# Kernel optimization log

Measured on AMD Instinct MI355X. Metric: run time of the kernel, lower is better.

## Reference

```python
import jax, jax.numpy as jnp
import numpy as np

SEQ_LEN = 4096
EMBED_DIM = 1280
NUM_HEADS = 16
HEAD_DIM = EMBED_DIM // NUM_HEADS  # 80
SCALING = float(np.sqrt(HEAD_DIM))  # NOTE: source multiplies by sqrt(head_dim)
NEG_INF = float(np.finfo(np.float32).min)


def rotate_half(x):
    x1, x2 = jnp.split(x, 2, axis=-1)
    return jnp.concatenate((-x2, x1), axis=-1)


def setup_inputs() -> dict:
    key = jax.random.key(0)
    ks = jax.random.split(key, 7)
    s = 0.02
    hidden_states = jax.random.normal(ks[0], (SEQ_LEN, EMBED_DIM), dtype=jnp.float32)
    w_qkv = jax.random.normal(ks[1], (3 * EMBED_DIM, EMBED_DIM), dtype=jnp.float32) * s
    b_qkv = jax.random.normal(ks[2], (3 * EMBED_DIM,), dtype=jnp.float32) * s
    w_proj = jax.random.normal(ks[3], (EMBED_DIM, EMBED_DIM), dtype=jnp.float32) * s
    b_proj = jax.random.normal(ks[4], (EMBED_DIM,), dtype=jnp.float32) * s
    # rotary angles: theta duplicated to head_dim (emb = cat(rope, rope))
    inv_freq = 1.0 / (10000.0 ** (jnp.arange(0, HEAD_DIM // 2, dtype=jnp.float32) * 2.0 / HEAD_DIM))
    pos = jnp.arange(SEQ_LEN, dtype=jnp.float32)
    freqs = pos[:, None] * inv_freq[None, :]            # [S, hd/2]
    emb = jnp.concatenate((freqs, freqs), axis=-1)       # [S, hd]
    cos = jnp.cos(emb)
    sin = jnp.sin(emb)
    # 4 packed images of 1024 patches each
    cu_seqlens = jnp.array([0, 1024, 2048, 3072, 4096], dtype=jnp.int32)
    return {
        "hidden_states": hidden_states,
        "w_qkv": w_qkv, "b_qkv": b_qkv,
        "w_proj": w_proj, "b_proj": b_proj,
        "cos": cos, "sin": sin,
        "cu_seqlens": cu_seqlens,
    }


def reference(hidden_states, w_qkv, b_qkv, w_proj, b_proj, cos, sin, cu_seqlens):
    S = hidden_states.shape[0]
    # packed QKV projection
    qkv = hidden_states @ w_qkv.T + b_qkv                  # [S, 3D]
    qkv = qkv.reshape(S, 3, NUM_HEADS, HEAD_DIM)
    q, k, v = qkv[:, 0], qkv[:, 1], qkv[:, 2]              # [S, H, hd]
    # fp32 RoPE (broadcast cos/sin over heads)
    c = cos[:, None, :].astype(jnp.float32)
    sn = sin[:, None, :].astype(jnp.float32)
    qf, kf = q.astype(jnp.float32), k.astype(jnp.float32)
    q = (qf * c + rotate_half(qf) * sn).astype(q.dtype)
    k = (kf * c + rotate_half(kf) * sn).astype(k.dtype)
    # block-diagonal mask from cu_seqlens: same segment -> 0, else -inf
    pos = jnp.arange(S)
    seg = jnp.searchsorted(cu_seqlens, pos, side="right") - 1  # [S]
    bias = jnp.where(seg[:, None] == seg[None, :], 0.0, NEG_INF)  # [S, S]
    # dense attention over whole packed sequence (as in source)
    scores = jnp.einsum("shd,thd->hst", q, k) * SCALING + bias[None]
    weights = jax.nn.softmax(scores.astype(jnp.float32), axis=-1).astype(q.dtype)
    attn = jnp.einsum("hst,thd->shd", weights, v).reshape(S, EMBED_DIM)
    return attn @ w_proj.T + b_proj
```

## Files before the change

### kernel.cpp

```cpp
#include <hip/hip_runtime.h>

#define SEQ   4096
#define EMB   1280
#define NH    16
#define HD    80
#define HDP   96
#define O3    3840
#define SEGLEN 1024
#define NSEG  4
#define QSCALE (8.94427190999915878564f * 1.44269504088896340736f)

typedef unsigned short u16;
typedef __attribute__((ext_vector_type(8))) _Float16 f16x8;
typedef __attribute__((ext_vector_type(4))) _Float16 f16x4;
typedef __attribute__((ext_vector_type(2))) __fp16   h16x2;
typedef __attribute__((ext_vector_type(4))) float    f32x4;

__device__ __forceinline__ float ex2(float x) { return __builtin_amdgcn_exp2f(x); }

__device__ __forceinline__ u16 f2h(float f) {
  union { _Float16 h; u16 u; } v; v.h = (_Float16)f; return v.u;
}
__device__ __forceinline__ float h2f(u16 b) {
  union { u16 u; _Float16 h; } v; v.u = b; return (float)v.h;
}
__device__ __forceinline__ f32x4 exp2_4(f32x4 x) {
  f32x4 r; r.x = ex2(x.x); r.y = ex2(x.y); r.z = ex2(x.z); r.w = ex2(x.w); return r;
}
__device__ __forceinline__ f16x4 pk4(f32x4 s) {
  union { h16x2 h[2]; f16x4 f; } u;
  u.h[0] = __builtin_amdgcn_cvt_pkrtz(s.x, s.y);
  u.h[1] = __builtin_amdgcn_cvt_pkrtz(s.z, s.w);
  return u.f;
}
__device__ __forceinline__ void gl2lds16(const u16* g, u16* l) {
  __builtin_amdgcn_global_load_lds(
      (const __attribute__((address_space(1))) unsigned int*)g,
      (__attribute__((address_space(3))) unsigned int*)l, 16, 0, 0);
}

#define CVT_N1 (SEQ * EMB / 4)
#define CVT_N2 (O3 * EMB / 4)
#define CVT_N3 (EMB * EMB / 4)
__global__ void cvt_all_kernel(const float* __restrict__ a, const float* __restrict__ b,
                               const float* __restrict__ c, u16* __restrict__ oa,
                               u16* __restrict__ ob, u16* __restrict__ oc) {
  int i = blockIdx.x * blockDim.x + threadIdx.x;
  const float* src; u16* dst; int j = i;
  if (j < CVT_N1)                { src = a; dst = oa; }
  else if (j < CVT_N1 + CVT_N2)  { src = b; dst = ob; j -= CVT_N1; }
  else                           { src = c; dst = oc; j -= CVT_N1 + CVT_N2; }
  float4 f = ((const float4*)src)[j];
  union { u16 h[4]; uint2 v; } o;
  o.h[0] = f2h(f.x); o.h[1] = f2h(f.y); o.h[2] = f2h(f.z); o.h[3] = f2h(f.w);
  ((uint2*)dst)[j] = o.v;
}

template<int OUTF>
__global__ __launch_bounds__(256)
void gemm_bias_kernel(const u16* __restrict__ A, const u16* __restrict__ W,
                      const float* __restrict__ bias, void* __restrict__ Cout,
                      int N, int K) {
  __shared__ u16 As[128][64];
  __shared__ u16 Bs[128][64];
  const int tid  = threadIdx.x;
  const int bm   = blockIdx.y, bn = blockIdx.x;
  const int lane = tid & 63;
  const int wid  = tid >> 6;
  const int wm   = (wid >> 1) * 64, wn = (wid & 1) * 64;
  const int lr   = lane & 15, quad = lane >> 4;

  f32x4 acc[4][4];
  const f32x4 z4 = {0.f, 0.f, 0.f, 0.f};
  #pragma unroll
  for (int i = 0; i < 4; ++i)
    #pragma unroll
    for (int j = 0; j < 4; ++j) acc[i][j] = z4;

  const int arow = tid >> 3;
  const int acol = (((tid & 7) ^ (arow & 7)) * 8);
  const u16* Ab = A + (size_t)(bm * 128) * K;
  const u16* Wb = W + (size_t)(bn * 128) * K;
  u16* AsL = &As[0][0] + tid * 8;
  u16* BsL = &Bs[0][0] + tid * 8;

  for (int kt = 0; kt < K; kt += 64) {
    #pragma unroll
    for (int r = 0; r < 4; ++r) {
      gl2lds16(&Ab[(size_t)(arow + r * 32) * K + kt + acol], AsL + r * 2048);
      gl2lds16(&Wb[(size_t)(arow + r * 32) * K + kt + acol], BsL + r * 2048);
    }
    __syncthreads();
    #pragma unroll
    for (int k32 = 0; k32 < 2; ++k32) {
      const int c = (((k32 * 4 + quad) ^ (lr & 7)) * 8);
      f16x8 aF[4], bF[4];
      #pragma unroll
      for (int i = 0; i < 4; ++i) {
        aF[i] = *(const f16x8*)&As[wm + i * 16 + lr][c];
        bF[i] = *(const f16x8*)&Bs[wn + i * 16 + lr][c];
      }
      #pragma unroll
      for (int i = 0; i < 4; ++i)
        #pragma unroll
        for (int j = 0; j < 4; ++j)
          acc[i][j] = __builtin_amdgcn_mfma_f32_16x16x32_f16(aF[i], bF[j], acc[i][j], 0, 0, 0);
    }
    __syncthreads();
  }

  #pragma unroll
  for (int i = 0; i < 4; ++i) {
    int rowb = bm * 128 + wm + i * 16 + quad * 4;
    #pragma unroll
    for (int j = 0; j < 4; ++j) {
      int col = bn * 128 + wn + j * 16 + lr;
      float bv = bias[col];
      #pragma unroll
      for (int r = 0; r < 4; ++r) {
        float v = acc[i][j][r] + bv;
        if (OUTF) ((float*)Cout)[(size_t)(rowb + r) * N + col] = v;
        else      ((u16*)Cout)[(size_t)(rowb + r) * N + col] = f2h(v);
      }
    }
  }
}

__global__ __launch_bounds__(256)
void rope_reorg_kernel(const u16* __restrict__ qkv, const float* __restrict__ cosp,
                       const float* __restrict__ sinp, u16* __restrict__ Qp,
                       u16* __restrict__ Kp, u16* __restrict__ Vt) {
  __shared__ u16 Qs[64][80];
  __shared__ u16 Ks[64][80];
  __shared__ u16 Vs[64][88];
  const int tid = threadIdx.x;
  const int s0 = blockIdx.x * 64;
  const int h  = blockIdx.y;

  for (int t = tid; t < 640; t += 256) {
    int r = t / 10, c = (t % 10) * 8;
    size_t g = (size_t)(s0 + r) * O3 + h * HD + c;
    *(uint4*)&Qs[r][c] = *(const uint4*)&qkv[g];
    *(uint4*)&Ks[r][c] = *(const uint4*)&qkv[g + EMB];
    *(uint4*)&Vs[r][c] = *(const uint4*)&qkv[g + 2 * EMB];
  }
  __syncthreads();

  for (int t = tid; t < 64 * 24; t += 256) {
    int r = t / 24, d4 = (t % 24) * 4;
    int s = s0 + r;
    size_t po = ((size_t)h * SEQ + s) * HDP + d4;
    if (d4 >= HD) {
      uint2 z = make_uint2(0, 0);
      *(uint2*)&Qp[po] = z; *(uint2*)&Kp[po] = z;
      continue;
    }
    float4 cv = *(const float4*)&cosp[(size_t)s * HD + d4];
    float4 sv = *(const float4*)&sinp[(size_t)s * HD + d4];
    int dp4 = (d4 < 40) ? d4 + 40 : d4 - 40;
    float sgn = (d4 < 40) ? -1.f : 1.f;
    union { u16 h[4]; uint2 v; } oq, ok;
    const float* cp = (const float*)&cv;
    const float* sp = (const float*)&sv;
    #pragma unroll
    for (int j = 0; j < 4; ++j) {
      float q  = h2f(Qs[r][d4 + j]),  k  = h2f(Ks[r][d4 + j]);
      float qp = h2f(Qs[r][dp4 + j]), kp = h2f(Ks[r][dp4 + j]);
      oq.h[j] = f2h((q * cp[j] + sgn * qp * sp[j]) * QSCALE);
      ok.h[j] = f2h(k * cp[j] + sgn * kp * sp[j]);
    }
    *(uint2*)&Qp[po] = oq.v;
    *(uint2*)&Kp[po] = ok.v;
  }

  for (int t = tid; t < HD * 8; t += 256) {
    int d = t / 8, sc = (t % 8) * 8;
    union { u16 h[8]; uint4 v; } o;
    #pragma unroll
    for (int j = 0; j < 8; ++j) o.h[j] = Vs[sc + j][d];
    *(uint4*)&Vt[((size_t)(h * HD + d)) * SEQ + s0 + sc] = o.v;
  }
}

__global__ __launch_bounds__(256)
void attn_kernel(const u16* __restrict__ Qp, const u16* __restrict__ Kp,
                 const u16* __restrict__ Vt, u16* __restrict__ attnO) {
  __shared__ u16 K_l[64][96];
  __shared__ u16 V_l[80][64];

  const int tid = threadIdx.x;
  const int lane = tid & 63, w = tid >> 6;
  const int lr = lane & 15, quad = lane >> 4;
  const int h = blockIdx.y, sg = blockIdx.z;
  const int seg0 = sg * SEGLEN;
  const int q0b = seg0 + blockIdx.x * 64;

  f16x8 qF[3];
  {
    int qrow = q0b + w * 16 + lr;
    #pragma unroll
    for (int kc = 0; kc < 3; ++kc)
      qF[kc] = *(const f16x8*)&Qp[((size_t)h * SEQ + qrow) * HDP + kc * 32 + quad * 8];
  }

  const u16* Kbase = Kp + ((size_t)h * SEQ + seg0) * HDP;
  const u16* Vbase = Vt + (size_t)h * HD * SEQ + seg0;
  const u16* pK[3]; u16* dK[3];
  const u16* pV[3]; u16* dV[3];
  #pragma unroll
  for (int t = 0; t < 3; ++t) {
    int s = t * 256 + tid;
    int r = s / 12, c = s % 12;
    pK[t] = Kbase + (size_t)r * HDP + c * 8;
    dK[t] = &K_l[0][0] + s * 8;
    int rv = s / 8, cv = s % 8;
    int cg = cv ^ (rv & 7);
    pV[t] = Vbase + (size_t)rv * SEQ + cg * 8;
    dV[t] = &V_l[0][0] + s * 8;
  }

  const f32x4 z4 = {0.f, 0.f, 0.f, 0.f};
  float m_r = -3.0e38f;
  float l_r = 0.0f;
  f32x4 Oacc[5];
  #pragma unroll
  for (int n = 0; n < 5; ++n) Oacc[n] = z4;

  for (int kt = 0; kt < SEGLEN; kt += 64) {
    gl2lds16(pK[0], dK[0]); gl2lds16(pK[1], dK[1]); gl2lds16(pK[2], dK[2]);
    gl2lds16(pV[0], dV[0]); gl2lds16(pV[1], dV[1]);
    if (tid < 128) gl2lds16(pV[2], dV[2]);
    #pragma unroll
    for (int t = 0; t < 3; ++t) { pK[t] += 64 * HDP; pV[t] += 64; }
    __syncthreads();

    f32x4 S[4];
    #pragma unroll
    for (int ct = 0; ct < 4; ++ct) {
      S[ct] = z4;
      #pragma unroll
      for (int kc = 0; kc < 3; ++kc) {
        f16x8 kF = *(const f16x8*)&K_l[ct * 16 + lr][kc * 32 + quad * 8];
        S[ct] = __builtin_amdgcn_mfma_f32_16x16x32_f16(kF, qF[kc], S[ct], 0, 0, 0);
      }
    }

    float mx = fmaxf(fmaxf(S[0].x, S[0].y), fmaxf(S[0].z, S[0].w));
    #pragma unroll
    for (int ct = 1; ct < 4; ++ct)
      mx = fmaxf(mx, fmaxf(fmaxf(S[ct].x, S[ct].y), fmaxf(S[ct].z, S[ct].w)));
    mx = fmaxf(mx, __shfl_xor(mx, 16, 64));
    mx = fmaxf(mx, __shfl_xor(mx, 32, 64));
    float mnew = fmaxf(m_r, mx);
    float alpha = ex2(m_r - mnew);
    m_r = mnew;

    f32x4 mv = {mnew, mnew, mnew, mnew};
    float rs = 0.f;
    #pragma unroll
    for (int ct = 0; ct < 4; ++ct) {
      S[ct] = exp2_4(S[ct] - mv);
      rs += (S[ct].x + S[ct].y) + (S[ct].z + S[ct].w);
    }
    rs += __shfl_xor(rs, 16, 64);
    rs += __shfl_xor(rs, 32, 64);
    l_r = l_r * alpha + rs;

    if (__ballot(alpha != 1.0f)) {
      f32x4 al;
      al.x = __shfl(alpha, quad * 4 + 0, 64);
      al.y = __shfl(alpha, quad * 4 + 1, 64);
      al.z = __shfl(alpha, quad * 4 + 2, 64);
      al.w = __shfl(alpha, quad * 4 + 3, 64);
      #pragma unroll
      for (int n = 0; n < 5; ++n) Oacc[n] *= al;
    }

    f16x4 pF[4];
    #pragma unroll
    for (int ct = 0; ct < 4; ++ct) pF[ct] = pk4(S[ct]);

    #pragma unroll
    for (int ct = 0; ct < 4; ++ct) {
      const int cchunk = 2 * ct + (quad >> 1);
      #pragma unroll
      for (int n = 0; n < 5; ++n) {
        int vrow = n * 16 + lr;
        const u16* vp = &V_l[0][0] + vrow * 64 + ((cchunk ^ (vrow & 7)) << 3) + ((quad & 1) << 2);
        f16x4 vF = *(const f16x4*)vp;
        Oacc[n] = __builtin_amdgcn_mfma_f32_16x16x16f16(pF[ct], vF, Oacc[n], 0, 0, 0);
      }
    }
    __syncthreads();
  }

  f32x4 linv;
  linv.x = 1.0f / __shfl(l_r, quad * 4 + 0, 64);
  linv.y = 1.0f / __shfl(l_r, quad * 4 + 1, 64);
  linv.z = 1.0f / __shfl(l_r, quad * 4 + 2, 64);
  linv.w = 1.0f / __shfl(l_r, quad * 4 + 3, 64);
  #pragma unroll
  for (int n = 0; n < 5; ++n) {
    int rowb = q0b + w * 16 + quad * 4;
    int col = h * HD + n * 16 + lr;
    attnO[(size_t)(rowb + 0) * EMB + col] = f2h(Oacc[n].x * linv.x);
    attnO[(size_t)(rowb + 1) * EMB + col] = f2h(Oacc[n].y * linv.y);
    attnO[(size_t)(rowb + 2) * EMB + col] = f2h(Oacc[n].z * linv.z);
    attnO[(size_t)(rowb + 3) * EMB + col] = f2h(Oacc[n].w * linv.w);
  }
}

extern "C" void kernel_launch(void* const* d_in, const int* in_sizes, int n_in,
                              void* d_out, int out_size, void* d_ws, size_t ws_size,
                              hipStream_t stream) {
  const float* hs     = (const float*)d_in[0];
  const float* w_qkv  = (const float*)d_in[1];
  const float* b_qkv  = (const float*)d_in[2];
  const float* w_proj = (const float*)d_in[3];
  const float* b_proj = (const float*)d_in[4];
  const float* cosp   = (const float*)d_in[5];
  const float* sinp   = (const float*)d_in[6];
  float* out = (float*)d_out;

  char* p = (char*)d_ws;
  auto take = [&](size_t bytes) { char* q = p; p += (bytes + 255) & ~(size_t)255; return q; };
  u16* hsH    = (u16*)take((size_t)SEQ * EMB * 2);
  u16* wqkvH  = (u16*)take((size_t)O3 * EMB * 2);
  u16* wprojH = (u16*)take((size_t)EMB * EMB * 2);
  u16* qkvO   = (u16*)take((size_t)SEQ * O3 * 2);
  u16* Qp     = (u16*)take((size_t)NH * SEQ * HDP * 2);
  u16* Kp     = (u16*)take((size_t)NH * SEQ * HDP * 2);
  u16* Vt     = (u16*)take((size_t)NH * HD * SEQ * 2);
  u16* attnH  = (u16*)take((size_t)SEQ * EMB * 2);

  int ncvt = (CVT_N1 + CVT_N2 + CVT_N3) / 256;
  cvt_all_kernel<<<ncvt, 256, 0, stream>>>(hs, w_qkv, w_proj, hsH, wqkvH, wprojH);

  gemm_bias_kernel<0><<<dim3(O3 / 128, SEQ / 128), 256, 0, stream>>>(hsH, wqkvH, b_qkv, qkvO, O3, EMB);

  rope_reorg_kernel<<<dim3(SEQ / 64, NH), 256, 0, stream>>>(qkvO, cosp, sinp, Qp, Kp, Vt);

  attn_kernel<<<dim3(SEGLEN / 64, NH, NSEG), 256, 0, stream>>>(Qp, Kp, Vt, attnH);

  gemm_bias_kernel<1><<<dim3(EMB / 128, SEQ / 128), 256, 0, stream>>>(attnH, wprojH, b_proj, out, EMB, EMB);
}
```

Baseline: 254.3 us.

## Add 256x256-tile double-buffered GEMM kernel for QKV projection

After: 244.2 us. 4.0% less time.

```diff
diff --git a/kernel.cpp b/kernel.cpp
--- a/kernel.cpp
+++ b/kernel.cpp
@@ -126,6 +126,111 @@
   }
 }
 
+__global__ __launch_bounds__(512, 2)
+void gemm256_kernel(const u16* __restrict__ A, const u16* __restrict__ W,
+                    const float* __restrict__ bias, u16* __restrict__ Cout,
+                    int N, int K) {
+  __shared__ u16 As[2][256][64];
+  __shared__ u16 Bs[2][256][64];
+  const int tid  = threadIdx.x;
+  const int bm   = blockIdx.y, bn = blockIdx.x;
+  const int lane = tid & 63;
+  const int wid  = tid >> 6;
+  const int wm   = wid >> 2;
+  const int wn   = wid & 3;
+  const int lr   = lane & 15, quad = lane >> 4;
+  const int NT   = K >> 6;
+
+  const u16* Ab = A + (size_t)(bm * 256) * K;
+  const u16* Wb = W + (size_t)(bn * 256) * K;
+
+  const int srr  = tid >> 3;
+  const int scol = ((tid & 7) ^ (srr & 7)) << 3;
+  const u16* ApL = Ab + (size_t)srr * K + scol;
+  const u16* WpL = Wb + (size_t)srr * K + scol;
+
+  auto stA = [&](int b, int row0, int t) {
+    gl2lds16(ApL + (size_t)row0 * K + t * 64,        &As[b][row0][0]      + tid * 8);
+    gl2lds16(ApL + (size_t)(row0 + 64) * K + t * 64, &As[b][row0 + 64][0] + tid * 8);
+  };
+  auto stB = [&](int b, int row0, int t) {
+    gl2lds16(WpL + (size_t)row0 * K + t * 64,        &Bs[b][row0][0]      + tid * 8);
+    gl2lds16(WpL + (size_t)(row0 + 64) * K + t * 64, &Bs[b][row0 + 64][0] + tid * 8);
+  };
+
+  f32x4 acc[8][4];
+  const f32x4 z4 = {0.f, 0.f, 0.f, 0.f};
+  #pragma unroll
+  for (int i = 0; i < 8; ++i)
+    #pragma unroll
+    for (int j = 0; j < 4; ++j) acc[i][j] = z4;
+
+  stA(0, 0, 0); stA(0, 128, 0);
+  stB(0, 0, 0); stB(0, 128, 0);
+  stA(1, 0, 1);
+  asm volatile("s_waitcnt vmcnt(2)" ::: "memory");
+  __builtin_amdgcn_s_barrier();
+
+  for (int t = 0; t < NT; ++t) {
+    const int buf = t & 1, nb = buf ^ 1;
+    #pragma unroll
+    for (int mq = 0; mq < 2; ++mq) {
+      #pragma unroll
+      for (int k32 = 0; k32 < 2; ++k32) {
+        const int c = (((k32 * 4 + quad) ^ (lr & 7)) << 3);
+        f16x8 aF[4], bF[4];
+        #pragma unroll
+        for (int i = 0; i < 4; ++i)
+          aF[i] = *(const f16x8*)&As[buf][mq * 128 + wm * 64 + i * 16 + lr][c];
+        #pragma unroll
+        for (int j = 0; j < 4; ++j)
+          bF[j] = *(const f16x8*)&Bs[buf][wn * 64 + j * 16 + lr][c];
+        __builtin_amdgcn_sched_barrier(0);
+        if (mq == 0 && k32 == 0) {
+          if (t + 1 < NT) { stB(nb, 0, t + 1); stA(nb, 128, t + 1); }
+        } else if (mq == 0 && k32 == 1) {
+          if (t + 1 < NT) stB(nb, 128, t + 1);
+        } else if (mq == 1 && k32 == 0) {
+          if (t + 2 < NT) stA(buf, 0, t + 2);
+        }
+        __builtin_amdgcn_s_barrier();
+        asm volatile("s_waitcnt lgkmcnt(0)" ::: "memory");
+        __builtin_amdgcn_sched_barrier(0);
+        __builtin_amdgcn_s_setprio(1);
+        #pragma unroll
+        for (int i = 0; i < 4; ++i)
+          #pragma unroll
+          for (int j = 0; j < 4; ++j)
+            acc[mq * 4 + i][j] =
+                __builtin_amdgcn_mfma_f32_16x16x32_f16(aF[i], bF[j], acc[mq * 4 + i][j], 0, 0, 0);
+        __builtin_amdgcn_s_setprio(0);
+        if (mq == 1 && k32 == 1) {
+          if (t < NT - 2) asm volatile("s_waitcnt vmcnt(2)" ::: "memory");
+          else            asm volatile("s_waitcnt vmcnt(0)" ::: "memory");
+        }
+        __builtin_amdgcn_s_barrier();
+        __builtin_amdgcn_sched_barrier(0);
+      }
+    }
+  }
+
+  #pragma unroll
+  for (int mq = 0; mq < 2; ++mq) {
+    #pragma unroll
+    for (int i = 0; i < 4; ++i) {
+      const int rowb = bm * 256 + mq * 128 + wm * 64 + i * 16 + quad * 4;
+      #pragma unroll
+      for (int j = 0; j < 4; ++j) {
+        const int col = bn * 256 + wn * 64 + j * 16 + lr;
+        const float bv = bias[col];
+        #pragma unroll
+        for (int r = 0; r < 4; ++r)
+          Cout[(size_t)(rowb + r) * N + col] = f2h(acc[mq * 4 + i][j][r] + bv);
+      }
+    }
+  }
+}
+
 __global__ __launch_bounds__(256)
 void rope_reorg_kernel(const u16* __restrict__ qkv, const float* __restrict__ cosp,
                        const float* __restrict__ sinp, u16* __restrict__ Qp,
@@ -336,7 +441,7 @@
   int ncvt = (CVT_N1 + CVT_N2 + CVT_N3) / 256;
   cvt_all_kernel<<<ncvt, 256, 0, stream>>>(hs, w_qkv, w_proj, hsH, wqkvH, wprojH);
 
-  gemm_bias_kernel<0><<<dim3(O3 / 128, SEQ / 128), 256, 0, stream>>>(hsH, wqkvH, b_qkv, qkvO, O3, EMB);
+  gemm256_kernel<<<dim3(O3 / 256, SEQ / 256), 512, 0, stream>>>(hsH, wqkvH, b_qkv, qkvO, O3, EMB);
 
   rope_reorg_kernel<<<dim3(SEQ / 64, NH), 256, 0, stream>>>(qkvO, cosp, sinp, Qp, Kp, Vt);
 
```
